# Kernel tuning notes

Measured on AMD Instinct MI355X. Metric: run time of the kernel, lower is better.

## Reference

```python
import jax, jax.numpy as jnp
import numpy as np

T = 1048576      # signal length
K = 3            # number of IMFs
ALPHA = 2000.0   # bandwidth penalty
TAU = 1e-7       # dual ascent step
TOL = 1e-6       # convergence tolerance
N_ITER = 50      # max fixed-point iterations


def _vmd(x, omega_init):
    T_ = x.shape[0]
    t = jnp.arange(1, T_ + 1, dtype=jnp.float32) / T_
    freqs = t - 0.5 - 1.0 / T_                           # [T]
    f_hat = jnp.fft.fftshift(jnp.fft.fft(x))             # [T] complex
    u0 = jnp.zeros((K, T_), dtype=f_hat.dtype)
    lam0 = jnp.zeros((T_,), dtype=f_hat.dtype)

    def step(carry, n):
        u_prev, lam_prev, omega, done = carry
        base = (freqs[None, :] - omega[:, None]) ** 2    # [K,T]
        # mode k's denom also gets (freqs-omega[k-1])^2 and (freqs-omega[k+1])^2
        nbr = jnp.zeros_like(base).at[1:].add(base[:-1]).at[:-1].add(base[1:])
        denom = base + nbr + TAU ** 2
        u_hat = (f_hat[None, :] - lam_prev[None, :] / 2.0) / (1.0 + ALPHA * denom)
        pw = jnp.real(u_hat) ** 2 + jnp.imag(u_hat) ** 2  # |u_hat|^2, [K,T]
        omega_new = jnp.sum(freqs[None, :] * pw, axis=1) / jnp.sum(pw, axis=1)
        lam_new = lam_prev + TAU * (jnp.sum(u_hat, axis=0) - f_hat)
        # convergence check (every 10th iter), mirrors the original break
        u_diff = jnp.sum(jnp.abs(u_hat - u_prev) ** 2) / jnp.sum(jnp.abs(u_prev) ** 2)
        om_diff = jnp.sum(jnp.abs(omega_new - jnp.roll(omega_new, 1))) / K
        conv = (n % 10 == 0) & (u_diff < TOL) & (om_diff < TOL)
        # freeze state once converged (break-iteration's fresh u_hat is kept)
        u_out = jnp.where(done, u_prev, u_hat)
        lam_out = jnp.where(done, lam_prev, lam_new)
        om_out = jnp.where(done, omega, omega_new)
        return (u_out, lam_out, om_out, done | conv), None

    init = (u0, lam0, omega_init.astype(jnp.float32), jnp.array(False))
    (u_hat, _, _, _), _ = jax.lax.scan(jax.checkpoint(step), init, jnp.arange(N_ITER))
    imfs = jnp.real(jnp.fft.ifft(jnp.fft.ifftshift(u_hat, axes=-1), axis=-1))
    return imfs.astype(jnp.float32)                      # [K,T]


def setup_inputs() -> dict:
    key = jax.random.key(0)
    kx, ko = jax.random.split(key)
    x = jax.random.normal(kx, (T,), dtype=jnp.float32)
    omega_init = jax.random.uniform(ko, (K,), dtype=jnp.float32) * 0.5  # init==1
    return {"x": x, "omega_init": omega_init}


def reference(x, omega_init):
    return _vmd(x, omega_init)
```

## Files before the change

### kernel.cpp

```cpp
#include <hip/hip_runtime.h>
#include <math.h>


#define ALPHA_F 2000.0f

static __device__ __forceinline__ int lpad2(int i) { return i + (i >> 4); }
static __device__ __forceinline__ int swz(int i)  { return ((i & 7) << 7) | (i >> 3); }
static __device__ __forceinline__ int swzA(int i) { return ((i & 7) << 6) | (i >> 3); }
static __device__ __forceinline__ float frcp(float x) { return __builtin_amdgcn_rcpf(x); }

typedef float v2f __attribute__((ext_vector_type(2)));
static __device__ __forceinline__ v2f sp(float s) { v2f r; r.x = s; r.y = s; return r; }
static __device__ __forceinline__ v2f v2(float a, float b) { v2f r; r.x = a; r.y = b; return r; }
static __device__ __forceinline__ v2f pkfma(v2f a, v2f b, v2f c)
{ return __builtin_elementwise_fma(a, b, c); }
static __device__ __forceinline__ v2f cmul(v2f a, v2f w)
{
  v2f t = a * sp(w.x);
  v2f s = v2(-a.y, a.x);
  return pkfma(s, sp(w.y), t);
}
static __device__ __forceinline__ v2f cmulrr(v2f a, float wr, float wi)
{
  v2f t = a * sp(wr);
  v2f s = v2(-a.y, a.x);
  return pkfma(s, sp(wi), t);
}

#define PADN2 1088

template<int CTRL>
static __device__ __forceinline__ float dpp_addf(float v)
{
  int r = __builtin_amdgcn_update_dpp(0, __float_as_int(v), CTRL, 0xf, 0xf, true);
  return v + __int_as_float(r);
}
static __device__ __forceinline__ float wave64_sum(float v)
{
  v = dpp_addf<0x111>(v);
  v = dpp_addf<0x112>(v);
  v = dpp_addf<0x114>(v);
  v = dpp_addf<0x118>(v);
  v = dpp_addf<0x142>(v);
  v = dpp_addf<0x143>(v);
  return v;
}
static __device__ __forceinline__ float row8_sum(float v)
{
  v = dpp_addf<0x111>(v);
  v = dpp_addf<0x112>(v);
  v = dpp_addf<0x114>(v);
  return v;
}
static __device__ __forceinline__ float rdlane(float v, int l)
{
  return __int_as_float(__builtin_amdgcn_readlane(__float_as_int(v), l));
}

template<int SIGN>
static __device__ __forceinline__ void bfly4(v2f Y0, v2f Y1, v2f Y2, v2f Y3,
    float w1r, float w1i, float w2r, float w2i, float w3r, float w3i,
    v2f& o0, v2f& o1, v2f& o2, v2f& o3)
{
  v2f y1 = cmulrr(Y1, w1r, w1i), y2 = cmulrr(Y2, w2r, w2i),
      y3 = cmulrr(Y3, w3r, w3i);
  v2f t0 = Y0 + y2, t1 = Y0 - y2, t2 = y1 + y3, t3 = y1 - y3;
  o0 = t0 + t2; o2 = t0 - t2;
  v2f ns3 = v2(t3.y, -t3.x);
  if (SIGN < 0) { o1 = t1 + ns3; o3 = t1 - ns3; }
  else          { o1 = t1 - ns3; o3 = t1 + ns3; }
}
template<int SIGN>
static __device__ __forceinline__ void bfly4_nt(v2f X0, v2f X1, v2f X2, v2f X3,
    v2f& o0, v2f& o1, v2f& o2, v2f& o3)
{
  v2f t0 = X0 + X2, t1 = X0 - X2, t2 = X1 + X3, t3 = X1 - X3;
  o0 = t0 + t2; o2 = t0 - t2;
  v2f ns3 = v2(t3.y, -t3.x);
  if (SIGN < 0) { o1 = t1 + ns3; o3 = t1 - ns3; }
  else          { o1 = t1 - ns3; o3 = t1 + ns3; }
}

template<int SIGN>
static __device__ void fft1024p_reg(v2f X0, v2f X1, v2f X2, v2f X3,
                                    v2f* A, v2f* B)
{
  const int u = threadIdx.x;
  {
    v2f o0, o1, o2, o3;
    bfly4_nt<SIGN>(X0, X1, X2, X3, o0, o1, o2, o3);
    const int base = u << 2;
    B[lpad2(base    )] = o0; B[lpad2(base + 1)] = o1;
    B[lpad2(base + 2)] = o2; B[lpad2(base + 3)] = o3;
    __syncthreads();
  }
#pragma unroll
  for (int st = 1; st < 5; ++st) {
    v2f *in  = (st & 1) ? B : A;
    v2f *out = (st & 1) ? A : B;
    const int quarter = 1 << (2 * st);
    const int p = u & (quarter - 1);
    const int g = u >> (2 * st);

    float sw, cw;
    sincospif((float)(2 * p) * (1.0f / (float)(4 << (2 * st))), &sw, &cw);
    const float w1r = cw, w1i = (SIGN < 0) ? -sw : sw;
    const float w2r = w1r * w1r - w1i * w1i, w2i = 2.0f * w1r * w1i;
    const float w3r = w2r * w1r - w2i * w1i, w3i = w2r * w1i + w2i * w1r;

    v2f o0, o1, o2, o3;
    bfly4<SIGN>(in[lpad2(u)], in[lpad2(u + 256)],
                in[lpad2(u + 512)], in[lpad2(u + 768)],
                w1r, w1i, w2r, w2i, w3r, w3i, o0, o1, o2, o3);

    const int base = (g << (2 * st + 2)) + p;
    out[lpad2(base              )] = o0;
    out[lpad2(base +     quarter)] = o1;
    out[lpad2(base + 2 * quarter)] = o2;
    out[lpad2(base + 3 * quarter)] = o3;
    __syncthreads();
  }
}

template<int SIGN>
static __device__ void fft1024p_dual(const v2f X[4], const v2f Y[4],
                                     v2f* A1, v2f* B1, v2f* A2, v2f* B2)
{
  const int u = threadIdx.x;
  {
    v2f o0, o1, o2, o3, p0, p1, p2, p3;
    bfly4_nt<SIGN>(X[0], X[1], X[2], X[3], o0, o1, o2, o3);
    bfly4_nt<SIGN>(Y[0], Y[1], Y[2], Y[3], p0, p1, p2, p3);
    const int base = u << 2;
    B1[lpad2(base    )] = o0; B1[lpad2(base + 1)] = o1;
    B1[lpad2(base + 2)] = o2; B1[lpad2(base + 3)] = o3;
    B2[lpad2(base    )] = p0; B2[lpad2(base + 1)] = p1;
    B2[lpad2(base + 2)] = p2; B2[lpad2(base + 3)] = p3;
    __syncthreads();
  }
#pragma unroll
  for (int st = 1; st < 5; ++st) {
    v2f *in1  = (st & 1) ? B1 : A1, *out1 = (st & 1) ? A1 : B1;
    v2f *in2  = (st & 1) ? B2 : A2, *out2 = (st & 1) ? A2 : B2;
    const int quarter = 1 << (2 * st);
    const int p = u & (quarter - 1);
    const int g = u >> (2 * st);

    float sw, cw;
    sincospif((float)(2 * p) * (1.0f / (float)(4 << (2 * st))), &sw, &cw);
    const float w1r = cw, w1i = (SIGN < 0) ? -sw : sw;
    const float w2r = w1r * w1r - w1i * w1i, w2i = 2.0f * w1r * w1i;
    const float w3r = w2r * w1r - w2i * w1i, w3i = w2r * w1i + w2i * w1r;

    v2f o0, o1, o2, o3, p0, p1, p2, p3;
    bfly4<SIGN>(in1[lpad2(u)], in1[lpad2(u + 256)],
                in1[lpad2(u + 512)], in1[lpad2(u + 768)],
                w1r, w1i, w2r, w2i, w3r, w3i, o0, o1, o2, o3);
    bfly4<SIGN>(in2[lpad2(u)], in2[lpad2(u + 256)],
                in2[lpad2(u + 512)], in2[lpad2(u + 768)],
                w1r, w1i, w2r, w2i, w3r, w3i, p0, p1, p2, p3);

    const int base = (g << (2 * st + 2)) + p;
    out1[lpad2(base              )] = o0;
    out1[lpad2(base +     quarter)] = o1;
    out1[lpad2(base + 2 * quarter)] = o2;
    out1[lpad2(base + 3 * quarter)] = o3;
    out2[lpad2(base              )] = p0;
    out2[lpad2(base +     quarter)] = p1;
    out2[lpad2(base + 2 * quarter)] = p2;
    out2[lpad2(base + 3 * quarter)] = p3;
    __syncthreads();
  }
}

__global__ __launch_bounds__(256) void k_fwd_passA(const float* __restrict__ x,
                                                   float2* __restrict__ ws0)
{
  __shared__ __align__(16) v2f A[PADN2], B[PADN2];
  const int p = swzA(blockIdx.x);
  const int tid = threadIdx.x;
  const int c0 = 2 * p;
  v2f X[4];
#pragma unroll
  for (int q = 0; q < 4; ++q)
    X[q] = ((const v2f*)x)[(size_t)(tid + 256 * q) * 512 + p];
  fft1024p_reg<-1>(X[0], X[1], X[2], X[3], A, B);

  float sa, ca, sb, cb, ssa, cca, ssb, ccb;
  sincospif((float)(c0 * tid) * (2.0f / 1048576.0f), &sa, &ca);
  sincospif((float)((c0 + 1) * tid) * (2.0f / 1048576.0f), &sb, &cb);
  sincospif((float)c0 * (1.0f / 2048.0f), &ssa, &cca);
  sincospif((float)(c0 + 1) * (1.0f / 2048.0f), &ssb, &ccb);
  v2f E0 = v2(ca, -sa), E1 = v2(cb, -sb);
  const v2f S0 = v2(cca, -ssa), S1 = v2(ccb, -ssb);
#pragma unroll
  for (int q = 0; q < 2; ++q) {
    int k = tid + 256 * q;
    int kk = (1024 - k) & 1023;
    v2f Z = B[lpad2(k)];
    v2f Wv = B[lpad2(kk)];
    float X0r = 0.5f * (Z.x + Wv.x), X0i = 0.5f * (Z.y - Wv.y);
    float X1r = 0.5f * (Z.y + Wv.y), X1i = 0.5f * (Wv.x - Z.x);
    v2f o01 = cmul(v2(X0r, X0i), E0);
    v2f o23 = cmul(v2(X1r, X1i), E1);
    float4 o = make_float4(o01.x, o01.y, o23.x, o23.y);
    ((float4*)ws0)[(size_t)k * 512 + p] = o;
    if (q == 0) { E0 = cmul(E0, S0); E1 = cmul(E1, S1); }
  }
  if (tid == 0) {
    v2f Z = B[lpad2(512)];
    float s0, c0f, s1, c1f;
    sincospif((float)c0 * (1.0f / 1024.0f), &s0, &c0f);
    sincospif((float)(c0 + 1) * (1.0f / 1024.0f), &s1, &c1f);
    v2f o01 = cmul(v2(Z.x, 0.0f), v2(c0f, -s0));
    v2f o23 = cmul(v2(Z.y, 0.0f), v2(c1f, -s1));
    float4 o = make_float4(o01.x, o01.y, o23.x, o23.y);
    ((float4*)ws0)[(size_t)512 * 512 + p] = o;
  }
}

__global__ __launch_bounds__(256) void k_fwd_passB(const float2* __restrict__ ws0,
                                                   float2* __restrict__ fhat,
                                                   float* __restrict__ ET)
{
  __shared__ __align__(16) v2f A[PADN2], B[PADN2];
  const int b = blockIdx.x;
  const int tid = threadIdx.x;
  v2f X[4];
#pragma unroll
  for (int q = 0; q < 4; ++q)
    X[q] = ((const v2f*)ws0)[(size_t)b * 1024 + tid + 256 * q];
  fft1024p_reg<-1>(X[0], X[1], X[2], X[3], A, B);
  const bool mir = (b >= 1) && (b <= 511);
#pragma unroll
  for (int q = 0; q < 4; ++q) {
    int k2 = tid + 256 * q;
    v2f v = B[lpad2(k2)];
    float e = v.x * v.x + v.y * v.y;
    fhat[(size_t)b * 1024 + k2] = make_float2(v.x, v.y);
    ET[(size_t)k2 * 1024 + b] = e;
    if (mir) {
      fhat[(size_t)(1024 - b) * 1024 + (1023 - k2)] = make_float2(v.x, -v.y);
      ET[(size_t)(1023 - k2) * 1024 + (1024 - b)] = e;
    }
  }
}

static __device__ __forceinline__ void lag4(float x, float& l0, float& l1,
                                            float& l2, float& l3)
{
  float m0 = x, m1 = x - (1.0f / 3.0f), m2 = x - (2.0f / 3.0f), m3 = x - 1.0f;
  l0 = -4.5f * m1 * m2 * m3;
  l1 = 13.5f * m0 * m2 * m3;
  l2 = -13.5f * m0 * m1 * m3;
  l3 =  4.5f * m0 * m1 * m2;
}

__global__ __launch_bounds__(256) void k_moments(const float* __restrict__ ET,
                                                 double* __restrict__ W)
{
  __shared__ double red[4 * 4];
  const int B = blockIdx.x;
  const int k2 = B ^ 512;
  const int tid = threadIdx.x;
  double a0 = 0, a1 = 0, a2 = 0, a3 = 0;
#pragma unroll
  for (int q = 0; q < 4; ++q) {
    int k1 = tid + 256 * q;
    float e = ET[(size_t)k2 * 1024 + k1];
    float l0, l1, l2, l3;
    lag4((float)k1 * (1.0f / 1024.0f), l0, l1, l2, l3);
    a0 += (double)(e * l0); a1 += (double)(e * l1);
    a2 += (double)(e * l2); a3 += (double)(e * l3);
  }
  const int lane = tid & 63, wv = tid >> 6;
  double pv[4] = { a0, a1, a2, a3 };
#pragma unroll
  for (int j = 0; j < 4; ++j) {
    double v = pv[j];
    for (int off = 32; off; off >>= 1) v += __shfl_down(v, off, 64);
    if (lane == 0) red[wv * 4 + j] = v;
  }
  __syncthreads();
  if (tid < 4)
    W[B * 4 + tid] = red[tid] + red[4 + tid] + red[8 + tid] + red[12 + tid];
}

__global__ __launch_bounds__(512) void k_solve(
    const double* __restrict__ W4, const float* __restrict__ omega_init,
    float* __restrict__ omegaF)
{
  __shared__ float red[2][64];
  const int t = threadIdx.x;
  const int lane = t & 63, wv = t >> 6;

  float Wsc[8], fsc[8];
#pragma unroll
  for (int e = 0; e < 8; ++e) {
    Wsc[e] = (float)W4[t * 8 + e];
    int bin = 2 * t + (e >> 2);
    fsc[e] = (float)((double)bin / 1024.0 + (double)(e & 3) / 3072.0 - 0.5);
  }
  v2f frA[4], WrA[4], WfA[4];
#pragma unroll
  for (int i = 0; i < 4; ++i) {
    frA[i] = v2(fsc[2 * i], fsc[2 * i + 1]);
    WrA[i] = v2(Wsc[2 * i], Wsc[2 * i + 1]);
    WfA[i] = WrA[i] * frA[i];
  }
  float om0 = omega_init[0], om1 = omega_init[1], om2 = omega_init[2];

#pragma unroll 1
  for (int it = 0; it < 49; ++it) {
    float* rb = red[it & 1];
    v2f p0 = sp(0.f), p1 = sp(0.f), p2 = sp(0.f),
        p3 = sp(0.f), p4 = sp(0.f), p5 = sp(0.f);

#pragma unroll
    for (int i = 0; i < 4; ++i) {
      const v2f fv = frA[i];
      v2f a0 = fv - sp(om0), a1 = fv - sp(om1), a2 = fv - sp(om2);
      v2f t0 = sp(ALPHA_F) * a0, t1 = sp(ALPHA_F) * a1, t2 = sp(ALPHA_F) * a2;
      v2f m1 = pkfma(t1, a1, sp(1.0f));
      v2f dA = pkfma(t0, a0, m1);
      v2f dC = pkfma(t2, a2, m1);
      v2f dB = pkfma(t2, a2, dA);
      v2f AB = dA * dB, BC = dB * dC, AC = dA * dC;
      v2f ABC = AB * dC;
      float rr = frcp(ABC.x * ABC.y);
      v2f r = v2(rr * ABC.y, rr * ABC.x);
      v2f v0 = r * BC, v1 = r * AC, v2_ = r * AB;
      v2f g0 = v0 * v0, g1 = v1 * v1, g2 = v2_ * v2_;
      p0 = pkfma(WfA[i], g0, p0); p1 = pkfma(WfA[i], g1, p1);
      p2 = pkfma(WfA[i], g2, p2);
      p3 = pkfma(WrA[i], g0, p3); p4 = pkfma(WrA[i], g1, p4);
      p5 = pkfma(WrA[i], g2, p5);
    }

    float q0 = p0.x + p0.y, q1 = p1.x + p1.y, q2 = p2.x + p2.y;
    float q3 = p3.x + p3.y, q4 = p4.x + p4.y, q5 = p5.x + p5.y;

    q0 = wave64_sum(q0); q1 = wave64_sum(q1); q2 = wave64_sum(q2);
    q3 = wave64_sum(q3); q4 = wave64_sum(q4); q5 = wave64_sum(q5);
    if (lane == 63) {
      rb[0 * 8 + wv] = q0; rb[1 * 8 + wv] = q1; rb[2 * 8 + wv] = q2;
      rb[3 * 8 + wv] = q3; rb[4 * 8 + wv] = q4; rb[5 * 8 + wv] = q5;
    }
    __syncthreads();
    float v1r = red[it & 1][lane];
    v1r = row8_sum(v1r);
    float n0 = rdlane(v1r, 7),  n1 = rdlane(v1r, 15), n2 = rdlane(v1r, 23);
    float e0 = rdlane(v1r, 31), e1 = rdlane(v1r, 39), e2 = rdlane(v1r, 47);
    float ie01 = frcp(e0 * e1);
    om0 = n0 * (ie01 * e1);
    om1 = n1 * (ie01 * e0);
    om2 = n2 * frcp(e2);
  }

  if (t == 0) { omegaF[0] = om0; omegaF[1] = om1; omegaF[2] = om2; }
}

__global__ __launch_bounds__(256) void k_inv_A2(
    const float2* __restrict__ fhat, const float* __restrict__ omegaF,
    float2* __restrict__ ws0)
{
  __shared__ __align__(16) v2f A1[PADN2], B1[PADN2], A2[PADN2], B2[PADN2];
  const int tid = threadIdx.x;
  const int b = swz(blockIdx.x);
  const bool dual = (b <= 512);
  const float om0 = omegaF[0], om1 = omegaF[1], om2 = omegaF[2];

  v2f X[4];
  v2f Y[4];
#pragma unroll
  for (int q = 0; q < 4; ++q) {
    int j = tid + 256 * q;
    float2 f = fhat[(size_t)b * 1024 + j];
    int bin = j ^ 512;
    int tt = (bin << 10) | b;
    float freq = (float)tt * (1.0f / 1048576.0f) - 0.5f;
    v2f fpm = v2(freq, -freq);
    v2f A0 = fpm - sp(om0), A1v = fpm - sp(om1), A2v = fpm - sp(om2);
    v2f D0 = A0 * A0, D1 = A1v * A1v, D2 = A2v * A2v;
    v2f DA = pkfma(sp(ALPHA_F), D0 + D1, sp(1.0f));
    v2f DB = pkfma(sp(ALPHA_F), D2, DA);
    float rrA = frcp(DA.x * DA.y);
    float rrB = frcp(DB.x * DB.y);
    float Rr = 0.5f * (rrA * DA.y + rrA * DA.x);
    float Ri = 0.5f * (rrB * DB.y + rrB * DB.x);
    X[q] = cmul(v2(f.x, f.y), v2(Rr, Ri));
    if (dual) {
      v2f DC = pkfma(sp(ALPHA_F), D1 + D2, sp(1.0f));
      float rrC = frcp(DC.x * DC.y);
      float Rr2 = 0.5f * (rrC * DC.y + rrC * DC.x);
      Y[q] = v2(f.x, f.y) * sp(Rr2);
    }
  }

  float sa, ca, ss, cs;
  sincospif((float)(b * tid) * (2.0f / 1048576.0f), &sa, &ca);
  sincospif((float)b * (1.0f / 2048.0f), &ss, &cs);
  v2f E = v2(ca, sa);
  const v2f S = v2(cs, ss);

  if (dual) {
    fft1024p_dual<1>(X, Y, A1, B1, A2, B2);
    const bool mir = (b >= 1) && (b <= 511);
#pragma unroll
    for (int q = 0; q < 4; ++q) {
      int m1i = tid + 256 * q;
      v2f va = B1[lpad2(m1i)];
      v2f vb = B2[lpad2(m1i)];
      v2f oa = cmul(va, E);
      v2f ob = cmul(vb, E);
      ws0[(size_t)m1i * 1024 + b]           = make_float2(oa.x, oa.y);
      ws0[1048576 + (size_t)m1i * 1024 + b] = make_float2(ob.x, ob.y);
      if (mir)
        ws0[1048576 + (size_t)m1i * 1024 + (1024 - b)] = make_float2(ob.x, -ob.y);
      E = cmul(E, S);
    }
  } else {
    fft1024p_reg<1>(X[0], X[1], X[2], X[3], A1, B1);
#pragma unroll
    for (int q = 0; q < 4; ++q) {
      int m1i = tid + 256 * q;
      v2f va = B1[lpad2(m1i)];
      v2f oa = cmul(va, E);
      ws0[(size_t)m1i * 1024 + b] = make_float2(oa.x, oa.y);
      E = cmul(E, S);
    }
  }
}

__global__ __launch_bounds__(256) void k_inv_B2(const float2* __restrict__ ws0,
                                                float* __restrict__ out)
{
  __shared__ __align__(16) v2f A[PADN2], B[PADN2];
  const int tid = threadIdx.x;
  const float sc = 1.0f / 1048576.0f;

  if (blockIdx.x < 1024) {
    const int b = swz(blockIdx.x);
    v2f X[4];
#pragma unroll
    for (int q = 0; q < 4; ++q)
      X[q] = ((const v2f*)ws0)[(size_t)b * 1024 + tid + 256 * q];
    fft1024p_reg<1>(X[0], X[1], X[2], X[3], A, B);
#pragma unroll
    for (int q = 0; q < 4; ++q) {
      int m2 = tid + 256 * q;
      v2f v = B[lpad2(m2)];
      out[(size_t)m2 * 1024 + b]           = v.x * sc;
      out[1048576 + (size_t)m2 * 1024 + b] = v.y * sc;
    }
  } else {
    const int s = swzA(blockIdx.x - 1024);
    const int b0 = 2 * s, b1 = 2 * s + 1;
#pragma unroll
    for (int q = 0; q < 4; ++q) {
      int j = tid + 256 * q;
      A[lpad2(j)] = ((const v2f*)ws0)[1048576 + (size_t)b0 * 1024 + j];
      B[lpad2(j)] = ((const v2f*)ws0)[1048576 + (size_t)b1 * 1024 + j];
    }
    __syncthreads();
    v2f Z[4];
#pragma unroll
    for (int q = 0; q < 4; ++q) {
      int j = tid + 256 * q;
      int mj = (1024 - j) & 1023;
      v2f W0j = A[lpad2(j)], W0m = A[lpad2(mj)];
      v2f W1j = B[lpad2(j)], W1m = B[lpad2(mj)];
      float H0r = 0.5f * (W0j.x + W0m.x), H0i = 0.5f * (W0j.y - W0m.y);
      float H1r = 0.5f * (W1j.x + W1m.x), H1i = 0.5f * (W1j.y - W1m.y);
      Z[q] = v2(H0r - H1i, H0i + H1r);
    }
    __syncthreads();
    fft1024p_reg<1>(Z[0], Z[1], Z[2], Z[3], A, B);
#pragma unroll
    for (int q = 0; q < 4; ++q) {
      int m2 = tid + 256 * q;
      v2f v = B[lpad2(m2)];
      out[2097152 + (size_t)m2 * 1024 + b0] = v.x * sc;
      out[2097152 + (size_t)m2 * 1024 + b1] = v.y * sc;
    }
  }
}

extern "C" void kernel_launch(void* const* d_in, const int* in_sizes, int n_in,
                              void* d_out, int out_size, void* d_ws, size_t ws_size,
                              hipStream_t stream)
{
  (void)in_sizes; (void)n_in; (void)out_size; (void)ws_size;
  const float* x       = (const float*)d_in[0];
  const float* om_init = (const float*)d_in[1];
  float* out = (float*)d_out;

  char* w = (char*)d_ws;
  const size_t MB = 1024ull * 1024ull;
  float2* fhat     = (float2*)(w);
  float*  ET       = (float*)(w + 8 * MB);
  double* W4       = (double*)(w + 12 * MB);
  float*  omegaF   = (float*)(w + 12 * MB + 48 * 1024);
  float2* scratch  = (float2*)(w + 16 * MB);

  k_fwd_passA<<<512, 256, 0, stream>>>(x, scratch);
  k_fwd_passB<<<513, 256, 0, stream>>>(scratch, fhat, ET);
  k_moments<<<1024, 256, 0, stream>>>(ET, W4);
  k_solve<<<1, 512, 0, stream>>>(W4, om_init, omegaF);
  k_inv_A2<<<1024, 256, 0, stream>>>(fhat, omegaF, scratch);
  k_inv_B2<<<1536, 256, 0, stream>>>(scratch, out);
}
```

Measured before the change: 167.8 us.

## Split dual inverse FFT blocks into separate blocks and shrink solver to 256 threads

The inverse pass A kernel previously ran two FFTs (two planes) in one block for half the columns, using four shared buffers. It now launches 1537 single-FFT blocks, with plane-1 columns handled by extra blocks, which lowers shared memory per block and balances work across blocks. The serial omega solver now uses 256 threads, each holding 16 elements, so the cross-wave reduction has 4 partials instead of 8. The aim is better occupancy and load balance in the inverse pass, and cheaper per-iteration sync in the solver. The cost is more total blocks, and the f_hat reads for plane-1 columns are now done twice.

```diff
diff --git a/kernel.cpp b/kernel.cpp
--- a/kernel.cpp
+++ b/kernel.cpp
@@ -45,11 +45,10 @@
   v = dpp_addf<0x143>(v);
   return v;
 }
-static __device__ __forceinline__ float row8_sum(float v)
+static __device__ __forceinline__ float row4_sum(float v)
 {
   v = dpp_addf<0x111>(v);
   v = dpp_addf<0x112>(v);
-  v = dpp_addf<0x114>(v);
   return v;
 }
 static __device__ __forceinline__ float rdlane(float v, int l)
@@ -118,57 +117,6 @@
     out[lpad2(base +     quarter)] = o1;
     out[lpad2(base + 2 * quarter)] = o2;
     out[lpad2(base + 3 * quarter)] = o3;
-    __syncthreads();
-  }
-}
-
-template<int SIGN>
-static __device__ void fft1024p_dual(const v2f X[4], const v2f Y[4],
-                                     v2f* A1, v2f* B1, v2f* A2, v2f* B2)
-{
-  const int u = threadIdx.x;
-  {
-    v2f o0, o1, o2, o3, p0, p1, p2, p3;
-    bfly4_nt<SIGN>(X[0], X[1], X[2], X[3], o0, o1, o2, o3);
-    bfly4_nt<SIGN>(Y[0], Y[1], Y[2], Y[3], p0, p1, p2, p3);
-    const int base = u << 2;
-    B1[lpad2(base    )] = o0; B1[lpad2(base + 1)] = o1;
-    B1[lpad2(base + 2)] = o2; B1[lpad2(base + 3)] = o3;
-    B2[lpad2(base    )] = p0; B2[lpad2(base + 1)] = p1;
-    B2[lpad2(base + 2)] = p2; B2[lpad2(base + 3)] = p3;
-    __syncthreads();
-  }
-#pragma unroll
-  for (int st = 1; st < 5; ++st) {
-    v2f *in1  = (st & 1) ? B1 : A1, *out1 = (st & 1) ? A1 : B1;
-    v2f *in2  = (st & 1) ? B2 : A2, *out2 = (st & 1) ? A2 : B2;
-    const int quarter = 1 << (2 * st);
-    const int p = u & (quarter - 1);
-    const int g = u >> (2 * st);
-
-    float sw, cw;
-    sincospif((float)(2 * p) * (1.0f / (float)(4 << (2 * st))), &sw, &cw);
-    const float w1r = cw, w1i = (SIGN < 0) ? -sw : sw;
-    const float w2r = w1r * w1r - w1i * w1i, w2i = 2.0f * w1r * w1i;
-    const float w3r = w2r * w1r - w2i * w1i, w3i = w2r * w1i + w2i * w1r;
-
-    v2f o0, o1, o2, o3, p0, p1, p2, p3;
-    bfly4<SIGN>(in1[lpad2(u)], in1[lpad2(u + 256)],
-                in1[lpad2(u + 512)], in1[lpad2(u + 768)],
-                w1r, w1i, w2r, w2i, w3r, w3i, o0, o1, o2, o3);
-    bfly4<SIGN>(in2[lpad2(u)], in2[lpad2(u + 256)],
-                in2[lpad2(u + 512)], in2[lpad2(u + 768)],
-                w1r, w1i, w2r, w2i, w3r, w3i, p0, p1, p2, p3);
-
-    const int base = (g << (2 * st + 2)) + p;
-    out1[lpad2(base              )] = o0;
-    out1[lpad2(base +     quarter)] = o1;
-    out1[lpad2(base + 2 * quarter)] = o2;
-    out1[lpad2(base + 3 * quarter)] = o3;
-    out2[lpad2(base              )] = p0;
-    out2[lpad2(base +     quarter)] = p1;
-    out2[lpad2(base + 2 * quarter)] = p2;
-    out2[lpad2(base + 3 * quarter)] = p3;
     __syncthreads();
   }
 }
@@ -286,7 +234,7 @@
     W[B * 4 + tid] = red[tid] + red[4 + tid] + red[8 + tid] + red[12 + tid];
 }
 
-__global__ __launch_bounds__(512) void k_solve(
+__global__ __launch_bounds__(256) void k_solve(
     const double* __restrict__ W4, const float* __restrict__ omega_init,
     float* __restrict__ omegaF)
 {
@@ -294,16 +242,16 @@
   const int t = threadIdx.x;
   const int lane = t & 63, wv = t >> 6;
 
-  float Wsc[8], fsc[8];
-#pragma unroll
-  for (int e = 0; e < 8; ++e) {
-    Wsc[e] = (float)W4[t * 8 + e];
-    int bin = 2 * t + (e >> 2);
+  float Wsc[16], fsc[16];
+#pragma unroll
+  for (int e = 0; e < 16; ++e) {
+    Wsc[e] = (float)W4[t * 16 + e];
+    int bin = 4 * t + (e >> 2);
     fsc[e] = (float)((double)bin / 1024.0 + (double)(e & 3) / 3072.0 - 0.5);
   }
-  v2f frA[4], WrA[4], WfA[4];
-#pragma unroll
-  for (int i = 0; i < 4; ++i) {
+  v2f frA[8], WrA[8], WfA[8];
+#pragma unroll
+  for (int i = 0; i < 8; ++i) {
     frA[i] = v2(fsc[2 * i], fsc[2 * i + 1]);
     WrA[i] = v2(Wsc[2 * i], Wsc[2 * i + 1]);
     WfA[i] = WrA[i] * frA[i];
@@ -317,7 +265,7 @@
         p3 = sp(0.f), p4 = sp(0.f), p5 = sp(0.f);
 
 #pragma unroll
-    for (int i = 0; i < 4; ++i) {
+    for (int i = 0; i < 8; ++i) {
       const v2f fv = frA[i];
       v2f a0 = fv - sp(om0), a1 = fv - sp(om1), a2 = fv - sp(om2);
       v2f t0 = sp(ALPHA_F) * a0, t1 = sp(ALPHA_F) * a1, t2 = sp(ALPHA_F) * a2;
@@ -343,14 +291,14 @@
     q0 = wave64_sum(q0); q1 = wave64_sum(q1); q2 = wave64_sum(q2);
     q3 = wave64_sum(q3); q4 = wave64_sum(q4); q5 = wave64_sum(q5);
     if (lane == 63) {
-      rb[0 * 8 + wv] = q0; rb[1 * 8 + wv] = q1; rb[2 * 8 + wv] = q2;
-      rb[3 * 8 + wv] = q3; rb[4 * 8 + wv] = q4; rb[5 * 8 + wv] = q5;
+      rb[0 * 4 + wv] = q0; rb[1 * 4 + wv] = q1; rb[2 * 4 + wv] = q2;
+      rb[3 * 4 + wv] = q3; rb[4 * 4 + wv] = q4; rb[5 * 4 + wv] = q5;
     }
     __syncthreads();
     float v1r = red[it & 1][lane];
-    v1r = row8_sum(v1r);
-    float n0 = rdlane(v1r, 7),  n1 = rdlane(v1r, 15), n2 = rdlane(v1r, 23);
-    float e0 = rdlane(v1r, 31), e1 = rdlane(v1r, 39), e2 = rdlane(v1r, 47);
+    v1r = row4_sum(v1r);
+    float n0 = rdlane(v1r, 3),  n1 = rdlane(v1r, 7),  n2 = rdlane(v1r, 11);
+    float e0 = rdlane(v1r, 15), e1 = rdlane(v1r, 19), e2 = rdlane(v1r, 23);
     float ie01 = frcp(e0 * e1);
     om0 = n0 * (ie01 * e1);
     om1 = n1 * (ie01 * e0);
@@ -364,14 +312,14 @@
     const float2* __restrict__ fhat, const float* __restrict__ omegaF,
     float2* __restrict__ ws0)
 {
-  __shared__ __align__(16) v2f A1[PADN2], B1[PADN2], A2[PADN2], B2[PADN2];
+  __shared__ __align__(16) v2f A[PADN2], B[PADN2];
   const int tid = threadIdx.x;
-  const int b = swz(blockIdx.x);
-  const bool dual = (b <= 512);
+  const int bb = blockIdx.x;
+  const bool pl1 = (bb >= 1024);
+  const int b = pl1 ? ((bb == 1536) ? 512 : swzA(bb - 1024)) : swz(bb);
   const float om0 = omegaF[0], om1 = omegaF[1], om2 = omegaF[2];
 
   v2f X[4];
-  v2f Y[4];
 #pragma unroll
   for (int q = 0; q < 4; ++q) {
     int j = tid + 256 * q;
@@ -382,20 +330,22 @@
     v2f fpm = v2(freq, -freq);
     v2f A0 = fpm - sp(om0), A1v = fpm - sp(om1), A2v = fpm - sp(om2);
     v2f D0 = A0 * A0, D1 = A1v * A1v, D2 = A2v * A2v;
-    v2f DA = pkfma(sp(ALPHA_F), D0 + D1, sp(1.0f));
-    v2f DB = pkfma(sp(ALPHA_F), D2, DA);
-    float rrA = frcp(DA.x * DA.y);
-    float rrB = frcp(DB.x * DB.y);
-    float Rr = 0.5f * (rrA * DA.y + rrA * DA.x);
-    float Ri = 0.5f * (rrB * DB.y + rrB * DB.x);
-    X[q] = cmul(v2(f.x, f.y), v2(Rr, Ri));
-    if (dual) {
+    if (!pl1) {
+      v2f DA = pkfma(sp(ALPHA_F), D0 + D1, sp(1.0f));
+      v2f DB = pkfma(sp(ALPHA_F), D2, DA);
+      float rrA = frcp(DA.x * DA.y);
+      float rrB = frcp(DB.x * DB.y);
+      float Rr = 0.5f * (rrA * DA.y + rrA * DA.x);
+      float Ri = 0.5f * (rrB * DB.y + rrB * DB.x);
+      X[q] = cmul(v2(f.x, f.y), v2(Rr, Ri));
+    } else {
       v2f DC = pkfma(sp(ALPHA_F), D1 + D2, sp(1.0f));
       float rrC = frcp(DC.x * DC.y);
       float Rr2 = 0.5f * (rrC * DC.y + rrC * DC.x);
-      Y[q] = v2(f.x, f.y) * sp(Rr2);
-    }
-  }
+      X[q] = v2(f.x, f.y) * sp(Rr2);
+    }
+  }
+  fft1024p_reg<1>(X[0], X[1], X[2], X[3], A, B);
 
   float sa, ca, ss, cs;
   sincospif((float)(b * tid) * (2.0f / 1048576.0f), &sa, &ca);
@@ -403,30 +353,25 @@
   v2f E = v2(ca, sa);
   const v2f S = v2(cs, ss);
 
-  if (dual) {
-    fft1024p_dual<1>(X, Y, A1, B1, A2, B2);
+  if (!pl1) {
+#pragma unroll
+    for (int q = 0; q < 4; ++q) {
+      int m1i = tid + 256 * q;
+      v2f va = B[lpad2(m1i)];
+      v2f oa = cmul(va, E);
+      ws0[(size_t)m1i * 1024 + b] = make_float2(oa.x, oa.y);
+      E = cmul(E, S);
+    }
+  } else {
     const bool mir = (b >= 1) && (b <= 511);
 #pragma unroll
     for (int q = 0; q < 4; ++q) {
       int m1i = tid + 256 * q;
-      v2f va = B1[lpad2(m1i)];
-      v2f vb = B2[lpad2(m1i)];
-      v2f oa = cmul(va, E);
+      v2f vb = B[lpad2(m1i)];
       v2f ob = cmul(vb, E);
-      ws0[(size_t)m1i * 1024 + b]           = make_float2(oa.x, oa.y);
       ws0[1048576 + (size_t)m1i * 1024 + b] = make_float2(ob.x, ob.y);
       if (mir)
         ws0[1048576 + (size_t)m1i * 1024 + (1024 - b)] = make_float2(ob.x, -ob.y);
-      E = cmul(E, S);
-    }
-  } else {
-    fft1024p_reg<1>(X[0], X[1], X[2], X[3], A1, B1);
-#pragma unroll
-    for (int q = 0; q < 4; ++q) {
-      int m1i = tid + 256 * q;
-      v2f va = B1[lpad2(m1i)];
-      v2f oa = cmul(va, E);
-      ws0[(size_t)m1i * 1024 + b] = make_float2(oa.x, oa.y);
       E = cmul(E, S);
     }
   }
@@ -506,7 +451,7 @@
   k_fwd_passA<<<512, 256, 0, stream>>>(x, scratch);
   k_fwd_passB<<<513, 256, 0, stream>>>(scratch, fhat, ET);
   k_moments<<<1024, 256, 0, stream>>>(ET, W4);
-  k_solve<<<1, 512, 0, stream>>>(W4, om_init, omegaF);
-  k_inv_A2<<<1024, 256, 0, stream>>>(fhat, omegaF, scratch);
+  k_solve<<<1, 256, 0, stream>>>(W4, om_init, omegaF);
+  k_inv_A2<<<1537, 256, 0, stream>>>(fhat, omegaF, scratch);
   k_inv_B2<<<1536, 256, 0, stream>>>(scratch, out);
 }
```

New measurement: 161.5 us. -3.8%, faster.
